# Kernel tuning notes

Measured on AMD Instinct MI355X. Metric: run time of the kernel, lower is better.

Reference implementation:

```python
import jax, jax.numpy as jnp
import numpy as np

LN_EPS = 1e-3   # keras LayerNormalization default epsilon
EPS = 1e-5      # module's self.eps
QB = 128.0      # 2**(bits-1) with bits=8


def ste_round(x):
    # straight-through round: forward = round(x), backward = identity
    return x + jax.lax.stop_gradient(jnp.round(x) - x)


def setup_inputs() -> dict:
    key = jax.random.key(0)
    k1, k2 = jax.random.split(key)
    x = jax.random.normal(k1, (4, 8192, 1024), dtype=jnp.float32)
    weight = jax.random.normal(k2, (1024, 1024), dtype=jnp.float32) * 0.02
    ln_gamma = jnp.ones((1024,), dtype=jnp.float32)
    ln_beta = jnp.zeros((1024,), dtype=jnp.float32)
    return {"x": x, "weight": weight, "ln_gamma": ln_gamma, "ln_beta": ln_beta}


def reference(x, weight, ln_gamma, ln_beta):
    # LayerNorm over last axis (keras defaults: eps=1e-3, learnable scale/center)
    mu = jnp.mean(x, axis=-1, keepdims=True)
    var = jnp.var(x, axis=-1, keepdims=True)
    xn = (x - mu) * jax.lax.rsqrt(var + LN_EPS) * ln_gamma + ln_beta

    # 1.58-bit weight ternarization with STE round
    beta = jnp.mean(jnp.abs(weight))                     # per-tensor scale
    w_q = jnp.clip(ste_round(weight / (beta + EPS)), -1.0, 1.0)

    # activation quantization (flg_before_linear=True branch)
    gamma = jnp.max(jnp.abs(xn))                         # per-tensor absmax
    xq = jnp.clip(xn * QB / gamma, -QB + EPS, QB - EPS)

    # quantized matmul + fused rescale
    y = jnp.einsum('bsd,du->bsu', xq, w_q)
    return y * (gamma * beta / QB)
```

## Files before the change

kernel.cpp:

```cpp
#include <hip/hip_runtime.h>
#include <hip/hip_bf16.h>
#include <stdint.h>


#define M_ROWS 32768
#define KDIM 1024
#define NDIM 1024

typedef int   v4i  __attribute__((ext_vector_type(4)));
typedef int   v16i __attribute__((ext_vector_type(16)));

__device__ __forceinline__ void async16(const void* g, void* l) {
    __builtin_amdgcn_global_load_lds((const __attribute__((address_space(1))) uint32_t*)g,
                                     (__attribute__((address_space(3))) uint32_t*)l,
                                     16, 0, 0);
}

__global__ __launch_bounds__(256) void absum_k(const float* __restrict__ w,
                                               float* __restrict__ partials) {
    int idx = blockIdx.x * 256 + threadIdx.x;
    float4 v = ((const float4*)w)[idx];
    float s = fabsf(v.x) + fabsf(v.y) + fabsf(v.z) + fabsf(v.w);
    #pragma unroll
    for (int o = 32; o; o >>= 1) s += __shfl_xor(s, o);
    __shared__ float p[4];
    if ((threadIdx.x & 63) == 0) p[threadIdx.x >> 6] = s;
    __syncthreads();
    if (threadIdx.x == 0) partials[blockIdx.x] = p[0] + p[1] + p[2] + p[3];
}

__global__ __launch_bounds__(256) void quant_k(const float* __restrict__ w,
                                               const float* __restrict__ partials,
                                               char* __restrict__ wqT,
                                               float* __restrict__ wsum) {
    int t = threadIdx.x;
    float s = partials[t] + partials[t + 256] + partials[t + 512] + partials[t + 768];
    #pragma unroll
    for (int o = 32; o; o >>= 1) s += __shfl_xor(s, o);
    __shared__ float ps[4];
    if ((t & 63) == 0) ps[t >> 6] = s;
    __syncthreads();
    float total = ps[0] + ps[1] + ps[2] + ps[3];
    if (blockIdx.x == 0 && t == 0) wsum[0] = total;
    float beta = total * (1.0f / 1048576.0f);
    float inv  = 1.0f / (beta + 1e-5f);

    __shared__ char sT[64 * 80];
    int k0 = (blockIdx.x >> 4) * 64, n0 = (blockIdx.x & 15) * 64;
    int n_l = t & 63;
    #pragma unroll
    for (int r = 0; r < 16; ++r) {
        int k_l = (t >> 6) * 16 + r;
        float q = rintf(w[(size_t)(k0 + k_l) * NDIM + n0 + n_l] * inv);
        q = fminf(1.0f, fmaxf(-1.0f, q));
        sT[n_l * 80 + k_l] = (char)(int)q;
    }
    __syncthreads();
    int nn = t >> 2, c = t & 3;
    v4i val = *(const v4i*)&sT[nn * 80 + c * 16];
    *(v4i*)&wqT[(size_t)(n0 + nn) * KDIM + k0 + c * 16] = val;
}

__global__ __launch_bounds__(256) void ln_q_k(const float* __restrict__ x,
                                              const float* __restrict__ g,
                                              const float* __restrict__ b,
                                              char* __restrict__ xq,
                                              float* __restrict__ rscale) {
    int tid = threadIdx.x;
    int lane = tid & 63;
    int row = blockIdx.x * 4 + (tid >> 6);
    const float4* xr = (const float4*)(x + (size_t)row * KDIM);
    float4 v[4];
    #pragma unroll
    for (int j = 0; j < 4; ++j) v[j] = xr[lane + 64 * j];
    float s = 0.f, ss = 0.f;
    #pragma unroll
    for (int j = 0; j < 4; ++j) {
        s  += v[j].x + v[j].y + v[j].z + v[j].w;
        ss += v[j].x * v[j].x + v[j].y * v[j].y + v[j].z * v[j].z + v[j].w * v[j].w;
    }
    #pragma unroll
    for (int o = 32; o; o >>= 1) { s += __shfl_xor(s, o); ss += __shfl_xor(ss, o); }
    float mu  = s * (1.0f / 1024.0f);
    float var = ss * (1.0f / 1024.0f) - mu * mu;
    float rs  = rsqrtf(var + 1e-3f);
    float xn[16];
    float mx = 0.f;
    #pragma unroll
    for (int j = 0; j < 4; ++j) {
        int p = lane + 64 * j;
        float4 gg = ((const float4*)g)[p];
        float4 bb = ((const float4*)b)[p];
        xn[4*j+0] = (v[j].x - mu) * rs * gg.x + bb.x;
        xn[4*j+1] = (v[j].y - mu) * rs * gg.y + bb.y;
        xn[4*j+2] = (v[j].z - mu) * rs * gg.z + bb.z;
        xn[4*j+3] = (v[j].w - mu) * rs * gg.w + bb.w;
        #pragma unroll
        for (int e = 0; e < 4; ++e) mx = fmaxf(mx, fabsf(xn[4*j+e]));
    }
    #pragma unroll
    for (int o = 32; o; o >>= 1) mx = fmaxf(mx, __shfl_xor(mx, o));
    mx = fmaxf(mx, 1e-20f);
    float scl = mx * (1.0f / 127.0f);
    float inv = 127.0f / mx;
    if (lane == 0) rscale[row] = scl;
    #pragma unroll
    for (int j = 0; j < 4; ++j) {
        char4 c;
        c.x = (char)(int)rintf(xn[4*j+0] * inv);
        c.y = (char)(int)rintf(xn[4*j+1] * inv);
        c.z = (char)(int)rintf(xn[4*j+2] * inv);
        c.w = (char)(int)rintf(xn[4*j+3] * inv);
        *(char4*)(xq + (size_t)row * KDIM + (lane + 64 * j) * 4) = c;
    }
}

__global__ __launch_bounds__(256) void gemm_k(const char* __restrict__ A,
                                              const char* __restrict__ B,
                                              const float* __restrict__ wsum,
                                              const float* __restrict__ rscale,
                                              float* __restrict__ out) {
    __shared__ char sA[128 * 128];
    __shared__ char sB[128 * 128];
    int tid = threadIdx.x;
    int w = tid >> 6, lane = tid & 63;
    int half = lane >> 5, l31 = lane & 31;
    int wm = w & 1, wn = w >> 1;
    int xcd   = blockIdx.x & 7;
    int local = blockIdx.x >> 3;
    int bm0 = (xcd * 32 + (local >> 3)) * 128;
    int bn0 = (local & 7) * 128;

    v16i acc[2][2] = {};

    int r_sub = lane >> 3;
    int p     = lane & 7;

    for (int kt = 0; kt < 8; ++kt) {
        int k0 = kt * 128;
        #pragma unroll
        for (int t = 0; t < 4; ++t) {
            int rb  = w * 32 + t * 8;
            int row = rb + r_sub;
            int c   = p ^ (row & 7);
            async16(A + (size_t)(bm0 + row) * KDIM + k0 + c * 16, &sA[rb * 128]);
            async16(B + (size_t)(bn0 + row) * KDIM + k0 + c * 16, &sB[rb * 128]);
        }
        __syncthreads();
        #pragma unroll
        for (int kk = 0; kk < 4; ++kk) {
            v4i af[2], bf[2];
            int c16 = kk * 2 + half;
            #pragma unroll
            for (int i = 0; i < 2; ++i) {
                int m = wm * 64 + i * 32 + l31;
                af[i] = *(const v4i*)&sA[m * 128 + (c16 ^ (m & 7)) * 16];
                int n = wn * 64 + i * 32 + l31;
                bf[i] = *(const v4i*)&sB[n * 128 + (c16 ^ (n & 7)) * 16];
            }
            #pragma unroll
            for (int i = 0; i < 2; ++i)
                #pragma unroll
                for (int j = 0; j < 2; ++j)
                    acc[i][j] = __builtin_amdgcn_mfma_i32_32x32x32_i8(af[i], bf[j], acc[i][j], 0, 0, 0);
        }
        __syncthreads();
    }

    float beta = wsum[0] * (1.0f / 1048576.0f);
    #pragma unroll
    for (int i = 0; i < 2; ++i) {
        #pragma unroll
        for (int r = 0; r < 16; ++r) {
            int mrow = bm0 + wm * 64 + i * 32 + (r & 3) + 8 * (r >> 2) + 4 * half;
            float sc = rscale[mrow] * beta;
            #pragma unroll
            for (int j = 0; j < 2; ++j) {
                int ncol = bn0 + wn * 64 + j * 32 + l31;
                out[(size_t)mrow * NDIM + ncol] = (float)acc[i][j][r] * sc;
            }
        }
    }
}

extern "C" void kernel_launch(void* const* d_in, const int* in_sizes, int n_in,
                              void* d_out, int out_size, void* d_ws, size_t ws_size,
                              hipStream_t stream) {
    const float* x        = (const float*)d_in[0];
    const float* weight   = (const float*)d_in[1];
    const float* ln_gamma = (const float*)d_in[2];
    const float* ln_beta  = (const float*)d_in[3];
    float* out = (float*)d_out;

    float* wsum     = (float*)d_ws;
    float* partials = (float*)((char*)d_ws + 4096);
    float* rscale   = (float*)((char*)d_ws + 8192);
    char*  wqT      = (char*)d_ws + (1u << 18);
    char*  xq       = (char*)d_ws + (1u << 21);

    absum_k<<<1024, 256, 0, stream>>>(weight, partials);
    quant_k<<<256, 256, 0, stream>>>(weight, partials, wqT, wsum);
    ln_q_k<<<M_ROWS / 4, 256, 0, stream>>>(x, ln_gamma, ln_beta, xq, rscale);
    gemm_k<<<(M_ROWS / 128) * (NDIM / 128), 256, 0, stream>>>(xq, wqT, wsum, rscale, out);
}
```

Measured before the change: 271.4 us.

## Enlarge int8 GEMM tile to 256x256 with triple-buffered async LDS pipeline

```diff
diff --git a/kernel.cpp b/kernel.cpp
--- a/kernel.cpp
+++ b/kernel.cpp
@@ -1,5 +1,4 @@
 #include <hip/hip_runtime.h>
-#include <hip/hip_bf16.h>
 #include <stdint.h>
 
 
@@ -9,6 +8,8 @@
 
 typedef int   v4i  __attribute__((ext_vector_type(4)));
 typedef int   v16i __attribute__((ext_vector_type(16)));
+
+#define MFMA_I8 __builtin_amdgcn_mfma_i32_32x32x32_i8
 
 __device__ __forceinline__ void async16(const void* g, void* l) {
     __builtin_amdgcn_global_load_lds((const __attribute__((address_space(1))) uint32_t*)g,
@@ -115,64 +116,91 @@
     }
 }
 
-__global__ __launch_bounds__(256) void gemm_k(const char* __restrict__ A,
+__global__ __launch_bounds__(512) void gemm_k(const char* __restrict__ A,
                                               const char* __restrict__ B,
                                               const float* __restrict__ wsum,
                                               const float* __restrict__ rscale,
                                               float* __restrict__ out) {
-    __shared__ char sA[128 * 128];
-    __shared__ char sB[128 * 128];
+    __shared__ char sA[3][16384];
+    __shared__ char sB[3][16384];
+
     int tid = threadIdx.x;
     int w = tid >> 6, lane = tid & 63;
     int half = lane >> 5, l31 = lane & 31;
-    int wm = w & 1, wn = w >> 1;
+    int wm = w >> 2, wn = w & 3;
+
     int xcd   = blockIdx.x & 7;
     int local = blockIdx.x >> 3;
-    int bm0 = (xcd * 32 + (local >> 3)) * 128;
-    int bn0 = (local & 7) * 128;
-
-    v16i acc[2][2] = {};
+    int bm0 = (xcd * 16 + (local >> 2)) * 256;
+    int bn0 = (local & 3) * 256;
 
     int r_sub = lane >> 3;
-    int p     = lane & 7;
-
-    for (int kt = 0; kt < 8; ++kt) {
-        int k0 = kt * 128;
+    int pc    = lane & 7;
+    int cch   = pc ^ r_sub;
+
+    int srl  = l31 >> 1;
+    int cb   = ((l31 & 1) << 2) | half;
+    int sxor = srl & 7;
+
+    #define STAGE(h, tt, bi) do { \
+        int hh_ = (h) & 1; \
+        int sr_ = hh_ * 64 + w * 8 + r_sub; \
+        int row_ = 2 * sr_ + (cch >> 2); \
+        size_t go_ = (size_t)row_ * KDIM + (tt) * 64 + (cch & 3) * 16; \
+        if ((h) < 2) async16(A + (size_t)bm0 * KDIM + go_, &sA[bi][hh_ * 8192 + w * 1024]); \
+        else         async16(B + (size_t)bn0 * KDIM + go_, &sB[bi][hh_ * 8192 + w * 1024]); \
+    } while (0)
+
+    v16i acc[4][2] = {};
+
+    #pragma unroll
+    for (int h = 0; h < 4; ++h) STAGE(h, 0, 0);
+    #pragma unroll
+    for (int h = 0; h < 4; ++h) STAGE(h, 1, 1);
+    asm volatile("s_waitcnt vmcnt(4)" ::: "memory");
+    __builtin_amdgcn_s_barrier();
+    __builtin_amdgcn_sched_barrier(0);
+
+    int rb = 0, wb = 2;
+    #pragma unroll 1
+    for (int t = 0; t < 16; ++t) {
+        const char* cA = sA[rb];
+        const char* cB = sB[rb];
         #pragma unroll
-        for (int t = 0; t < 4; ++t) {
-            int rb  = w * 32 + t * 8;
-            int row = rb + r_sub;
-            int c   = p ^ (row & 7);
-            async16(A + (size_t)(bm0 + row) * KDIM + k0 + c * 16, &sA[rb * 128]);
-            async16(B + (size_t)(bn0 + row) * KDIM + k0 + c * 16, &sB[rb * 128]);
+        for (int p = 0; p < 4; ++p) {
+            const int ipair = p & 1, kh = p >> 1;
+            int slot = ((cb | (kh << 1)) ^ sxor) << 4;
+            v4i af0 = *(const v4i*)&cA[(wm * 64 + (ipair * 2 + 0) * 16 + srl) * 128 + slot];
+            v4i af1 = *(const v4i*)&cA[(wm * 64 + (ipair * 2 + 1) * 16 + srl) * 128 + slot];
+            v4i bf0 = *(const v4i*)&cB[(wn * 32 +  0 + srl) * 128 + slot];
+            v4i bf1 = *(const v4i*)&cB[(wn * 32 + 16 + srl) * 128 + slot];
+            if (t < 14) STAGE(p, t + 2, wb);
+            __builtin_amdgcn_s_barrier();
+            __builtin_amdgcn_s_setprio(1);
+            acc[ipair * 2 + 0][0] = MFMA_I8(af0, bf0, acc[ipair * 2 + 0][0], 0, 0, 0);
+            acc[ipair * 2 + 0][1] = MFMA_I8(af0, bf1, acc[ipair * 2 + 0][1], 0, 0, 0);
+            acc[ipair * 2 + 1][0] = MFMA_I8(af1, bf0, acc[ipair * 2 + 1][0], 0, 0, 0);
+            acc[ipair * 2 + 1][1] = MFMA_I8(af1, bf1, acc[ipair * 2 + 1][1], 0, 0, 0);
+            __builtin_amdgcn_s_setprio(0);
+            __builtin_amdgcn_s_barrier();
         }
-        __syncthreads();
-        #pragma unroll
-        for (int kk = 0; kk < 4; ++kk) {
-            v4i af[2], bf[2];
-            int c16 = kk * 2 + half;
-            #pragma unroll
-            for (int i = 0; i < 2; ++i) {
-                int m = wm * 64 + i * 32 + l31;
-                af[i] = *(const v4i*)&sA[m * 128 + (c16 ^ (m & 7)) * 16];
-                int n = wn * 64 + i * 32 + l31;
-                bf[i] = *(const v4i*)&sB[n * 128 + (c16 ^ (n & 7)) * 16];
-            }
-            #pragma unroll
-            for (int i = 0; i < 2; ++i)
-                #pragma unroll
-                for (int j = 0; j < 2; ++j)
-                    acc[i][j] = __builtin_amdgcn_mfma_i32_32x32x32_i8(af[i], bf[j], acc[i][j], 0, 0, 0);
+        if (t < 15) {
+            if (t == 14) asm volatile("s_waitcnt vmcnt(0)" ::: "memory");
+            else         asm volatile("s_waitcnt vmcnt(4)" ::: "memory");
+            __builtin_amdgcn_s_barrier();
+            __builtin_amdgcn_sched_barrier(0);
         }
-        __syncthreads();
-    }
+        rb = (rb == 2) ? 0 : rb + 1;
+        wb = (wb == 2) ? 0 : wb + 1;
+    }
+    #undef STAGE
 
     float beta = wsum[0] * (1.0f / 1048576.0f);
     #pragma unroll
-    for (int i = 0; i < 2; ++i) {
+    for (int i = 0; i < 4; ++i) {
         #pragma unroll
         for (int r = 0; r < 16; ++r) {
-            int mrow = bm0 + wm * 64 + i * 32 + (r & 3) + 8 * (r >> 2) + 4 * half;
+            int mrow = bm0 + wm * 128 + i * 32 + (r & 3) + 8 * (r >> 2) + 4 * half;
             float sc = rscale[mrow] * beta;
             #pragma unroll
             for (int j = 0; j < 2; ++j) {
@@ -201,5 +229,5 @@
     absum_k<<<1024, 256, 0, stream>>>(weight, partials);
     quant_k<<<256, 256, 0, stream>>>(weight, partials, wqT, wsum);
     ln_q_k<<<M_ROWS / 4, 256, 0, stream>>>(x, ln_gamma, ln_beta, xq, rscale);
-    gemm_k<<<(M_ROWS / 128) * (NDIM / 128), 256, 0, stream>>>(xq, wqT, wsum, rscale, out);
-}
+    gemm_k<<<(M_ROWS / 256) * (NDIM / 256), 512, 0, stream>>>(xq, wqT, wsum, rscale, out);
+}
```

Result: slower. 288.1 us (+6.1%).
